# Performance work log

Measured on AMD Instinct MI355X. Metric: run time of the kernel, lower is better.

## Reference

```python
import jax, jax.numpy as jnp
import numpy as np
from functools import partial

H = 128      # hidden size
IN = 86      # lstm input size (66 pose + 20 conditioning)
OUT = 66     # decoded pose dims
STEPS = 15   # rollout steps


def lstm_cell(u, h, c, Wih, Whh, b):
    # PyTorch gate order: i, f, g, o ; b = b_ih + b_hh precombined by caller
    gates = u @ Wih.T + h @ Whh.T + b          # [B, 4H]
    i, f, g, o = jnp.split(gates, 4, axis=-1)
    i = jax.nn.sigmoid(i)
    f = jax.nn.sigmoid(f)
    g = jnp.tanh(g)
    o = jax.nn.sigmoid(o)
    c = f * c + i * g
    h = o * jnp.tanh(c)
    return h, c


def setup_inputs() -> dict:
    key = jax.random.key(0)
    ks = jax.random.split(key, 12)
    B, T = 8192, 50
    k = 1.0 / np.sqrt(H)  # torch default uniform init bound
    u = lambda kk, shp: jax.random.uniform(kk, shp, jnp.float32, -k, k)
    return {
        "x": jax.random.normal(ks[0], (B, T, IN), jnp.float32),
        "Wih0": u(ks[1], (4 * H, IN)),
        "Whh0": u(ks[2], (4 * H, H)),
        "bih0": u(ks[3], (4 * H,)),
        "bhh0": u(ks[4], (4 * H,)),
        "Wih1": u(ks[5], (4 * H, H)),
        "Whh1": u(ks[6], (4 * H, H)),
        "bih1": u(ks[7], (4 * H,)),
        "bhh1": u(ks[8], (4 * H,)),
        "Wd": u(ks[9], (OUT, H)),
        "bd": u(ks[10], (OUT,)),
    }


def reference(x, Wih0, Whh0, bih0, bhh0, Wih1, Whh1, bih1, bhh1, Wd, bd):
    B = x.shape[0]
    b0 = bih0 + bhh0
    b1 = bih1 + bhh1

    def two_layer(state, u):
        h1, c1, h2, c2 = state
        h1, c1 = lstm_cell(u, h1, c1, Wih0, Whh0, b0)
        h2, c2 = lstm_cell(h1, h2, c2, Wih1, Whh1, b1)
        return (h1, c1, h2, c2), h2

    z = jnp.zeros((B, H), x.dtype)
    state0 = (z, z, z, z)

    # encode the history sequence; only final (h, c) matter
    state, _ = jax.lax.scan(lambda s, u: (two_layer(s, u)[0], None),
                            state0, jnp.swapaxes(x, 0, 1))

    cond = x[:, -1, OUT:]  # [B, 20] conditioning, held fixed during rollout

    # first rollout step uses the full last input frame
    state, h2 = two_layer(state, x[:, -1, :])
    pose0 = h2 @ Wd.T + bd  # [B, 66]

    def roll(carry, _):
        state, pose = carry
        u = jnp.concatenate([pose, cond], axis=-1)  # [B, 86]
        state, h2 = two_layer(state, u)
        pose = h2 @ Wd.T + bd
        return (state, pose), pose

    (_, _), rest = jax.lax.scan(roll, (state, pose0), None, length=STEPS - 1)
    # rest: [14, B, 66] -> stack with pose0 along time
    out = jnp.concatenate([pose0[:, None, :], jnp.swapaxes(rest, 0, 1)], axis=1)
    return out  # [B, 15, 66]
```

## Files before the change

### kernel.cpp

```cpp
#include <hip/hip_runtime.h>
#include <cstdint>
#include <cstddef>

#define H_    128
#define IN_   86
#define OUT_  66
#define T_    50
#define B_    8192
#define NPOSE 15

#define K0T 7
#define K1T 8
#define KDT 4
#define NTD 5
#define S0  232
#define S1  264
#define BR  32
#define THR 512
#define RING 16

#define B0P_OFF 0
#define B0P_SZ  (K0T * 32 * 1024)
#define B1P_OFF (B0P_OFF + B0P_SZ)
#define B1P_SZ  (K1T * 32 * 1024)
#define BDP_OFF (B1P_OFF + B1P_SZ)
#define BDP_SZ  (KDT * NTD * 1024)
#define B0P_N (B0P_SZ / 2)
#define B1P_N (B1P_SZ / 2)
#define TOT_N ((B0P_SZ + B1P_SZ + BDP_SZ) / 2)

typedef __attribute__((ext_vector_type(8))) _Float16 hfrag;
typedef __attribute__((ext_vector_type(4))) float   ffrag;

#define MFMA16(AC, AA, BB) \
  AC = __builtin_amdgcn_mfma_f32_16x16x32_f16((AA), (BB), (AC), 0, 0, 0)

template <int N> struct IC { static constexpr int value = N; };
template <int N, class F>
__device__ __forceinline__ void cfor(F&& f) {
  if constexpr (N > 0) {
    cfor<N - 1>(static_cast<F&&>(f));
    f(IC<N - 1>{});
  }
}

template<int MODE>
constexpr int kt_of() { return MODE==0?15: MODE==1?12: MODE==2?8: MODE==3?3: 7; }

template <int N>
__device__ __forceinline__ void waitvm() {
  asm volatile("s_waitcnt vmcnt(%0)" :: "i"(N) : "memory");
}

__device__ __forceinline__ void gload_lds16(const void* g, void* l) {
  __builtin_amdgcn_global_load_lds(
      (const __attribute__((address_space(1))) unsigned int*)g,
      (__attribute__((address_space(3))) unsigned int*)l,
      16, 0, 0);
}

__device__ __forceinline__ unsigned short f16rn(float f) {
  union { _Float16 h; unsigned short u; } cv;
  cv.h = (_Float16)f;
  return cv.u;
}
__device__ __forceinline__ float sigmoid_f(float v) {
  return __fdividef(1.f, 1.f + __expf(-v));
}
__device__ __forceinline__ float tanh_f(float v) {
  float av = fabsf(v);
  float e  = __expf(-2.f * av);
  float t  = __fdividef(1.f - e, 1.f + e);
  return copysignf(t, v);
}

__global__ void wm_prep(
    const float* __restrict__ Wih0, const float* __restrict__ Whh0,
    const float* __restrict__ Wih1, const float* __restrict__ Whh1,
    const float* __restrict__ Wd,
    unsigned short* __restrict__ wsu)
{
  const int idx = blockIdx.x * 256 + threadIdx.x;
  if (idx >= TOT_N) return;
  int region, l;
  if (idx < B0P_N)               { region = 0; l = idx; }
  else if (idx < B0P_N + B1P_N)  { region = 1; l = idx - B0P_N; }
  else                           { region = 2; l = idx - (B0P_N + B1P_N); }

  int k, nt, lane, j;
  if (region < 2) {
    k  = l >> 14;
    int r1 = l & 16383;
    nt = r1 >> 9;
    int li = r1 & 511;
    lane = li >> 3; j = li & 7;
  } else {
    k  = l / 2560;
    int r1 = l % 2560;
    nt = r1 >> 9;
    int li = r1 & 511;
    lane = li >> 3; j = li & 7;
  }
  const int n  = nt * 16 + (lane & 15);
  const int kk = k * 32 + (lane >> 4) * 8 + j;

  float v = 0.f;
  if (region == 0) {
    if (kk < IN_)                    v = Wih0[n * IN_ + kk];
    else if (kk >= 96 && kk < 224)   v = Whh0[n * H_ + (kk - 96)];
  } else if (region == 1) {
    v = (kk < H_) ? Wih1[n * H_ + kk] : Whh1[n * H_ + (kk - H_)];
  } else {
    if (n < OUT_)                    v = Wd[n * H_ + kk];
  }
  wsu[idx] = f16rn(v);
}

__global__ __launch_bounds__(THR, 2) void wm_main(
    const float* __restrict__ x,
    const char*  __restrict__ wsb,
    const float* __restrict__ bih0, const float* __restrict__ bhh0,
    const float* __restrict__ bih1, const float* __restrict__ bhh1,
    const float* __restrict__ bd,
    float* __restrict__ out)
{
  __shared__ __align__(16) unsigned short A0h[BR * S0];
  __shared__ __align__(16) unsigned short A1h[BR * S1];
  __shared__ __align__(16) char RG[8][RING * 1024];

  const int tid  = threadIdx.x;
  const int lane = tid & 63;
  const int uw   = tid >> 6;
  const int ln15 = lane & 15;
  const int quad = lane >> 4;
  const int quad4 = quad * 4;
  const int lane16 = lane * 16;

  const char* B0 = wsb + B0P_OFF;
  const char* B1 = wsb + B1P_OFF;
  const char* BD = wsb + BDP_OFF;
  char* myring = &RG[uw][0];
  const _Float16* A0f = (const _Float16*)A0h;
  const _Float16* A1f = (const _Float16*)A1h;

  for (int i = tid; i < BR * S0; i += THR) A0h[i] = 0;
  for (int i = tid; i < BR * S1; i += THR) A1h[i] = 0;

  float b0r[4], b1r[4];
  #pragma unroll
  for (int g = 0; g < 4; ++g) {
    const int n = g * 128 + uw * 16 + ln15;
    b0r[g] = bih0[n] + bhh0[n];
    b1r[g] = bih1[n] + bhh1[n];
  }
  const int od = uw * 16 + ln15;
  const float bdr = (uw < NTD && od < OUT_) ? bd[od] : 0.f;

  float c1[2][4], c2[2][4];
  #pragma unroll
  for (int m = 0; m < 2; ++m)
    #pragma unroll
    for (int r = 0; r < 4; ++r) { c1[m][r] = 0.f; c2[m][r] = 0.f; }

  const int a0b0 = ln15 * S0 + quad * 8;
  const int a0b1 = (16 + ln15) * S0 + quad * 8;
  const int a1b0 = ln15 * S1 + quad * 8;
  const int a1b1 = (16 + ln15) * S1 + quad * 8;
  const int unit = uw * 16 + ln15;
  const int xr_row = tid >> 4;
  const int xr_col = tid & 15;

  ffrag acc0[2][4], acc1[2][4];

  auto binit0 = [&]() {
    #pragma unroll
    for (int m = 0; m < 2; ++m)
      #pragma unroll
      for (int g = 0; g < 4; ++g) acc0[m][g] = (ffrag){b0r[g], b0r[g], b0r[g], b0r[g]};
  };
  auto binit1 = [&]() {
    #pragma unroll
    for (int m = 0; m < 2; ++m)
      #pragma unroll
      for (int g = 0; g < 4; ++g) acc1[m][g] = (ffrag){b1r[g], b1r[g], b1r[g], b1r[g]};
  };
  auto pw_l1 = [&]() {
    #pragma unroll
    for (int m = 0; m < 2; ++m)
      #pragma unroll
      for (int rr = 0; rr < 4; ++rr) {
        const float ig = sigmoid_f(acc0[m][0][rr]);
        const float fg = sigmoid_f(acc0[m][1][rr]);
        const float gg = tanh_f(acc0[m][2][rr]);
        const float og = sigmoid_f(acc0[m][3][rr]);
        const float c  = fmaf(fg, c1[m][rr], ig * gg);
        c1[m][rr] = c;
        const float h  = og * tanh_f(c);
        const unsigned short hv = f16rn(h);
        const int row = m * 16 + quad4 + rr;
        A0h[row * S0 + 96 + unit] = hv;
        A1h[row * S1 + unit]      = hv;
      }
  };
  auto pw_l2 = [&]() {
    #pragma unroll
    for (int m = 0; m < 2; ++m)
      #pragma unroll
      for (int rr = 0; rr < 4; ++rr) {
        const float ig = sigmoid_f(acc1[m][0][rr]);
        const float fg = sigmoid_f(acc1[m][1][rr]);
        const float gg = tanh_f(acc1[m][2][rr]);
        const float og = sigmoid_f(acc1[m][3][rr]);
        const float c  = fmaf(fg, c2[m][rr], ig * gg);
        c2[m][rr] = c;
        const float h  = og * tanh_f(c);
        const int row = m * 16 + quad4 + rr;
        A1h[row * S1 + 128 + unit] = f16rn(h);
      }
  };

  auto issue_jt = [&](auto mc2, auto jc2) {
    constexpr int MODE = decltype(mc2)::value;
    constexpr int i = decltype(jc2)::value;
    constexpr bool i1 = (MODE <= 2) && (i < K1T);
    constexpr int ik = MODE==0 ? (i1 ? i : i - 8)
                     : MODE==1 ? (i1 ? i : 3 + (i - 8))
                     : i;
    constexpr int ISB = (4 * i) % RING;
    const char* src = (i1 ? B1 : B0) + (size_t)ik * 32 * 1024;
    #pragma unroll
    for (int g = 0; g < 4; ++g)
      gload_lds16(src + (size_t)(g * 8 + uw) * 1024 + lane16,
                  myring + (ISB + g) * 1024);
  };
  auto prefetch_g = [&](auto mc2) {
    constexpr int MODE = decltype(mc2)::value;
    constexpr int NP = kt_of<MODE>() < 4 ? kt_of<MODE>() : 4;
    cfor<NP>([&](auto jc) { issue_jt(mc2, jc); });
  };

  auto run_gemm = [&](auto mc, auto pfc) {
    constexpr int MODE = decltype(mc)::value;
    constexpr bool PF = decltype(pfc)::value != 0;
    constexpr int KT = kt_of<MODE>();
    if constexpr (!PF) prefetch_g(mc);
    cfor<KT>([&](auto jc) {
      constexpr int j = decltype(jc)::value;
      constexpr bool is1 = (MODE <= 2) && (j < K1T);
      constexpr int k = MODE==0 ? (is1 ? j : j - 8)
                      : MODE==1 ? (is1 ? j : 3 + (j - 8))
                      : j;
      constexpr int REM = KT - 1 - j;
      constexpr int W = 4 * (REM < 3 ? REM : 3);
      waitvm<W>();
      hfrag a0, a1;
      if constexpr (is1) {
        a0 = *(const hfrag*)(A1f + a1b0 + k * 32);
        a1 = *(const hfrag*)(A1f + a1b1 + k * 32);
      } else {
        a0 = *(const hfrag*)(A0f + a0b0 + k * 32);
        a1 = *(const hfrag*)(A0f + a0b1 + k * 32);
      }
      constexpr int SB = (4 * j) % RING;
      __builtin_amdgcn_s_setprio(1);
      #pragma unroll
      for (int g = 0; g < 4; ++g) {
        const hfrag bh = *(const hfrag*)(myring + (SB + g) * 1024 + lane16);
        if constexpr (is1) { MFMA16(acc1[0][g], a0, bh); MFMA16(acc1[1][g], a1, bh); }
        else               { MFMA16(acc0[0][g], a0, bh); MFMA16(acc0[1][g], a1, bh); }
      }
      __builtin_amdgcn_s_setprio(0);
      if constexpr (j + 4 < KT) issue_jt(mc, IC<j + 4>{});
    });
  };

  auto barrier2 = [&]() {
    asm volatile("s_waitcnt lgkmcnt(0)" ::: "memory");
    __builtin_amdgcn_s_barrier();
    asm volatile("" ::: "memory");
  };

  barrier2();

  {
    const float* xr = x + ((size_t)(blockIdx.x * BR + xr_row) * T_ + 0) * IN_;
    float xv[6];
    #pragma unroll
    for (int m = 0; m < 6; ++m) {
      const int k = xr_col + m * 16;
      xv[m] = (k < IN_) ? __builtin_nontemporal_load(xr + k) : 0.f;
    }
    #pragma unroll
    for (int m = 0; m < 6; ++m) {
      const int k = xr_col + m * 16;
      if (k < IN_) A0h[xr_row * S0 + k] = f16rn(xv[m]);
    }
  }
  prefetch_g(IC<4>{});
  barrier2();
  binit0();
  run_gemm(IC<4>{}, IC<1>{});
  barrier2();

  for (int t = 0; t < T_; ++t) {
    float xv[6];
    const bool stg = (t < T_ - 1);
    if (stg) {
      const float* xr = x + ((size_t)(blockIdx.x * BR + xr_row) * T_ + (t + 1)) * IN_;
      #pragma unroll
      for (int m = 0; m < 6; ++m) {
        const int k = xr_col + m * 16;
        xv[m] = (k < IN_) ? __builtin_nontemporal_load(xr + k) : 0.f;
      }
      __builtin_amdgcn_sched_barrier(0);
    }
    prefetch_g(IC<0>{});
    if (t > 0) pw_l2();
    pw_l1();
    if (stg) {
      #pragma unroll
      for (int m = 0; m < 6; ++m) {
        const int k = xr_col + m * 16;
        if (k < IN_) A0h[xr_row * S0 + k] = f16rn(xv[m]);
      }
    }
    barrier2();

    binit1();
    binit0();
    run_gemm(IC<0>{}, IC<1>{});
    barrier2();
  }

  for (int t = T_; t < T_ + NPOSE; ++t) {
    const bool more = (t < T_ + NPOSE - 1);
    prefetch_g(IC<2>{});
    if (t == T_) pw_l2();
    pw_l1();
    barrier2();

    binit1();
    if (more) { binit0(); run_gemm(IC<1>{}, IC<1>{}); }
    else      { run_gemm(IC<2>{}, IC<1>{}); }
    barrier2();

    hfrag bdreg[4];
    if (uw < NTD) {
      #pragma unroll
      for (int k = 0; k < KDT; ++k)
        bdreg[k] = *(const hfrag*)(BD + (size_t)(k * NTD + uw) * 1024 + lane16);
    }
    __builtin_amdgcn_sched_barrier(0);
    if (more) prefetch_g(IC<3>{});
    pw_l2();
    barrier2();

    const int s = t - T_;
    if (uw < NTD) {
      ffrag d0 = (ffrag){bdr, bdr, bdr, bdr};
      ffrag d1 = (ffrag){bdr, bdr, bdr, bdr};
      #pragma unroll
      for (int k = 0; k < KDT; ++k) {
        const hfrag ah0 = *(const hfrag*)(A1f + a1b0 + 128 + k * 32);
        const hfrag ah1 = *(const hfrag*)(A1f + a1b1 + 128 + k * 32);
        MFMA16(d0, ah0, bdreg[k]);
        MFMA16(d1, ah1, bdreg[k]);
      }
      if (od < OUT_) {
        #pragma unroll
        for (int m = 0; m < 2; ++m)
          #pragma unroll
          for (int rr = 0; rr < 4; ++rr) {
            const int row = m * 16 + quad4 + rr;
            const float v = m ? d1[rr] : d0[rr];
            __builtin_nontemporal_store(
                v, out + ((size_t)(blockIdx.x * BR + row) * NPOSE + s) * OUT_ + od);
            if (s < NPOSE - 1) A0h[row * S0 + od] = f16rn(v);
          }
      }
    }
    barrier2();

    if (more) run_gemm(IC<3>{}, IC<1>{});
  }
}

extern "C" void kernel_launch(void* const* d_in, const int* in_sizes, int n_in,
                              void* d_out, int out_size, void* d_ws, size_t ws_size,
                              hipStream_t stream)
{
  const float* x    = (const float*)d_in[0];
  const float* Wih0 = (const float*)d_in[1];
  const float* Whh0 = (const float*)d_in[2];
  const float* bih0 = (const float*)d_in[3];
  const float* bhh0 = (const float*)d_in[4];
  const float* Wih1 = (const float*)d_in[5];
  const float* Whh1 = (const float*)d_in[6];
  const float* bih1 = (const float*)d_in[7];
  const float* bhh1 = (const float*)d_in[8];
  const float* Wd   = (const float*)d_in[9];
  const float* bd   = (const float*)d_in[10];

  wm_prep<<<(TOT_N + 255) / 256, 256, 0, stream>>>(Wih0, Whh0, Wih1, Whh1, Wd,
                                                   (unsigned short*)d_ws);
  wm_main<<<B_ / BR, THR, 0, stream>>>(x, (const char*)d_ws,
                                       bih0, bhh0, bih1, bhh1, bd,
                                       (float*)d_out);
}
```

Before: 1.368 ms.

## Stream weight tiles directly into registers instead of an LDS ring

Replaces the per-wave LDS ring filled by async global_load_lds with a register-resident prefetch buffer of three k-tiles loaded by ordinary global loads. This removes the LDS round trip and the manual vmcnt waits, frees a large LDS allocation, and drops the sched_barriers so the compiler schedules the loads itself. The cost is higher VGPR pressure under launch bounds of two blocks per CU, a shallower prefetch depth, and waits on loads placed by the compiler.

```diff
diff --git a/kernel.cpp b/kernel.cpp
--- a/kernel.cpp
+++ b/kernel.cpp
@@ -17,7 +17,7 @@
 #define S1  264
 #define BR  32
 #define THR 512
-#define RING 16
+#define PF  3
 
 #define B0P_OFF 0
 #define B0P_SZ  (K0T * 32 * 1024)
@@ -46,18 +46,6 @@
 
 template<int MODE>
 constexpr int kt_of() { return MODE==0?15: MODE==1?12: MODE==2?8: MODE==3?3: 7; }
-
-template <int N>
-__device__ __forceinline__ void waitvm() {
-  asm volatile("s_waitcnt vmcnt(%0)" :: "i"(N) : "memory");
-}
-
-__device__ __forceinline__ void gload_lds16(const void* g, void* l) {
-  __builtin_amdgcn_global_load_lds(
-      (const __attribute__((address_space(1))) unsigned int*)g,
-      (__attribute__((address_space(3))) unsigned int*)l,
-      16, 0, 0);
-}
 
 __device__ __forceinline__ unsigned short f16rn(float f) {
   union { _Float16 h; unsigned short u; } cv;
@@ -126,7 +114,6 @@
 {
   __shared__ __align__(16) unsigned short A0h[BR * S0];
   __shared__ __align__(16) unsigned short A1h[BR * S1];
-  __shared__ __align__(16) char RG[8][RING * 1024];
 
   const int tid  = threadIdx.x;
   const int lane = tid & 63;
@@ -139,7 +126,6 @@
   const char* B0 = wsb + B0P_OFF;
   const char* B1 = wsb + B1P_OFF;
   const char* BD = wsb + BDP_OFF;
-  char* myring = &RG[uw][0];
   const _Float16* A0f = (const _Float16*)A0h;
   const _Float16* A1f = (const _Float16*)A1h;
 
@@ -171,6 +157,7 @@
   const int xr_col = tid & 15;
 
   ffrag acc0[2][4], acc1[2][4];
+  hfrag bp[PF][4];
 
   auto binit0 = [&]() {
     #pragma unroll
@@ -226,33 +213,30 @@
     constexpr int ik = MODE==0 ? (i1 ? i : i - 8)
                      : MODE==1 ? (i1 ? i : 3 + (i - 8))
                      : i;
-    constexpr int ISB = (4 * i) % RING;
+    constexpr int SLOT = i % PF;
     const char* src = (i1 ? B1 : B0) + (size_t)ik * 32 * 1024;
     #pragma unroll
     for (int g = 0; g < 4; ++g)
-      gload_lds16(src + (size_t)(g * 8 + uw) * 1024 + lane16,
-                  myring + (ISB + g) * 1024);
+      bp[SLOT][g] = *(const hfrag*)(src + (size_t)(g * 8 + uw) * 1024 + lane16);
   };
   auto prefetch_g = [&](auto mc2) {
     constexpr int MODE = decltype(mc2)::value;
-    constexpr int NP = kt_of<MODE>() < 4 ? kt_of<MODE>() : 4;
+    constexpr int NP = kt_of<MODE>() < PF ? kt_of<MODE>() : PF;
     cfor<NP>([&](auto jc) { issue_jt(mc2, jc); });
   };
 
   auto run_gemm = [&](auto mc, auto pfc) {
     constexpr int MODE = decltype(mc)::value;
-    constexpr bool PF = decltype(pfc)::value != 0;
+    constexpr bool PFD = decltype(pfc)::value != 0;
     constexpr int KT = kt_of<MODE>();
-    if constexpr (!PF) prefetch_g(mc);
+    if constexpr (!PFD) prefetch_g(mc);
     cfor<KT>([&](auto jc) {
       constexpr int j = decltype(jc)::value;
       constexpr bool is1 = (MODE <= 2) && (j < K1T);
       constexpr int k = MODE==0 ? (is1 ? j : j - 8)
                       : MODE==1 ? (is1 ? j : 3 + (j - 8))
                       : j;
-      constexpr int REM = KT - 1 - j;
-      constexpr int W = 4 * (REM < 3 ? REM : 3);
-      waitvm<W>();
+      constexpr int SLOT = j % PF;
       hfrag a0, a1;
       if constexpr (is1) {
         a0 = *(const hfrag*)(A1f + a1b0 + k * 32);
@@ -261,16 +245,14 @@
         a0 = *(const hfrag*)(A0f + a0b0 + k * 32);
         a1 = *(const hfrag*)(A0f + a0b1 + k * 32);
       }
-      constexpr int SB = (4 * j) % RING;
       __builtin_amdgcn_s_setprio(1);
       #pragma unroll
       for (int g = 0; g < 4; ++g) {
-        const hfrag bh = *(const hfrag*)(myring + (SB + g) * 1024 + lane16);
-        if constexpr (is1) { MFMA16(acc1[0][g], a0, bh); MFMA16(acc1[1][g], a1, bh); }
-        else               { MFMA16(acc0[0][g], a0, bh); MFMA16(acc0[1][g], a1, bh); }
+        if constexpr (is1) { MFMA16(acc1[0][g], a0, bp[SLOT][g]); MFMA16(acc1[1][g], a1, bp[SLOT][g]); }
+        else               { MFMA16(acc0[0][g], a0, bp[SLOT][g]); MFMA16(acc0[1][g], a1, bp[SLOT][g]); }
       }
       __builtin_amdgcn_s_setprio(0);
-      if constexpr (j + 4 < KT) issue_jt(mc, IC<j + 4>{});
+      if constexpr (j + PF < KT) issue_jt(mc, IC<j + PF>{});
     });
   };
 
@@ -312,7 +294,6 @@
         const int k = xr_col + m * 16;
         xv[m] = (k < IN_) ? __builtin_nontemporal_load(xr + k) : 0.f;
       }
-      __builtin_amdgcn_sched_barrier(0);
     }
     prefetch_g(IC<0>{});
     if (t > 0) pw_l2();
@@ -350,7 +331,6 @@
       for (int k = 0; k < KDT; ++k)
         bdreg[k] = *(const hfrag*)(BD + (size_t)(k * NTD + uw) * 1024 + lane16);
     }
-    __builtin_amdgcn_sched_barrier(0);
     if (more) prefetch_g(IC<3>{});
     pw_l2();
     barrier2();
```

Result: slower. 1.752 ms (+28.1%).

## Keep six layer-1 weight k-tiles resident in registers across timesteps

Applied to the files above, without the earlier changes.

Loads the first six k-tiles of the packed layer-1 weights into per-thread registers once, before the timestep loop. Each GEMM then runs those tiles straight from registers and streams only the remaining tiles through the LDS ring. Prefetch depth and ring size shrink from 4 to 3 stages, and two sched_barriers are removed. The aim is to cut global/L2 weight traffic and LDS ring pressure on every step, at the cost of 48 extra VGPRs per thread, which may lower occupancy or cause spills.

```diff
diff --git a/kernel.cpp b/kernel.cpp
--- a/kernel.cpp
+++ b/kernel.cpp
@@ -13,11 +13,12 @@
 #define K1T 8
 #define KDT 4
 #define NTD 5
+#define NW1 6
 #define S0  232
 #define S1  264
 #define BR  32
 #define THR 512
-#define RING 16
+#define RING 12
 
 #define B0P_OFF 0
 #define B0P_SZ  (K0T * 32 * 1024)
@@ -44,8 +45,18 @@
   }
 }
 
-template<int MODE>
-constexpr int kt_of() { return MODE==0?15: MODE==1?12: MODE==2?8: MODE==3?3: 7; }
+template<int MODE> constexpr int ns_of() {
+  return MODE==0?9: MODE==1?6: MODE==2?2: MODE==3?3: 7;
+}
+template<int MODE, int J> constexpr bool s_is1() {
+  return (MODE==0||MODE==1) ? (J<2) : (MODE==2);
+}
+template<int MODE, int J> constexpr int s_k() {
+  return MODE==0 ? (J<2 ? 6+J : J-2)
+       : MODE==1 ? (J<2 ? 6+J : J+1)
+       : MODE==2 ? 6+J
+       : J;
+}
 
 template <int N>
 __device__ __forceinline__ void waitvm() {
@@ -146,6 +157,14 @@
   for (int i = tid; i < BR * S0; i += THR) A0h[i] = 0;
   for (int i = tid; i < BR * S1; i += THR) A1h[i] = 0;
 
+  hfrag w1[NW1][4];
+  cfor<NW1>([&](auto kc) {
+    constexpr int kt = decltype(kc)::value;
+    #pragma unroll
+    for (int g = 0; g < 4; ++g)
+      w1[kt][g] = *(const hfrag*)(B1 + (size_t)((kt * 32 + g * 8 + uw) * 1024) + lane16);
+  });
+
   float b0r[4], b1r[4];
   #pragma unroll
   for (int g = 0; g < 4; ++g) {
@@ -222,10 +241,8 @@
   auto issue_jt = [&](auto mc2, auto jc2) {
     constexpr int MODE = decltype(mc2)::value;
     constexpr int i = decltype(jc2)::value;
-    constexpr bool i1 = (MODE <= 2) && (i < K1T);
-    constexpr int ik = MODE==0 ? (i1 ? i : i - 8)
-                     : MODE==1 ? (i1 ? i : 3 + (i - 8))
-                     : i;
+    constexpr bool i1 = s_is1<MODE, i>();
+    constexpr int ik = s_k<MODE, i>();
     constexpr int ISB = (4 * i) % RING;
     const char* src = (i1 ? B1 : B0) + (size_t)ik * 32 * 1024;
     #pragma unroll
@@ -235,42 +252,52 @@
   };
   auto prefetch_g = [&](auto mc2) {
     constexpr int MODE = decltype(mc2)::value;
-    constexpr int NP = kt_of<MODE>() < 4 ? kt_of<MODE>() : 4;
+    constexpr int NP = ns_of<MODE>() < 3 ? ns_of<MODE>() : 3;
     cfor<NP>([&](auto jc) { issue_jt(mc2, jc); });
   };
 
-  auto run_gemm = [&](auto mc, auto pfc) {
+  auto run_gemm = [&](auto mc) {
     constexpr int MODE = decltype(mc)::value;
-    constexpr bool PF = decltype(pfc)::value != 0;
-    constexpr int KT = kt_of<MODE>();
-    if constexpr (!PF) prefetch_g(mc);
-    cfor<KT>([&](auto jc) {
+    constexpr int NS = ns_of<MODE>();
+    if constexpr (MODE <= 2) {
+      cfor<NW1>([&](auto kc) {
+        constexpr int kt = decltype(kc)::value;
+        const hfrag a0 = *(const hfrag*)(A1f + a1b0 + kt * 32);
+        const hfrag a1v = *(const hfrag*)(A1f + a1b1 + kt * 32);
+        __builtin_amdgcn_s_setprio(1);
+        #pragma unroll
+        for (int g = 0; g < 4; ++g) {
+          MFMA16(acc1[0][g], a0, w1[kt][g]);
+          MFMA16(acc1[1][g], a1v, w1[kt][g]);
+        }
+        __builtin_amdgcn_s_setprio(0);
+      });
+    }
+    cfor<NS>([&](auto jc) {
       constexpr int j = decltype(jc)::value;
-      constexpr bool is1 = (MODE <= 2) && (j < K1T);
-      constexpr int k = MODE==0 ? (is1 ? j : j - 8)
-                      : MODE==1 ? (is1 ? j : 3 + (j - 8))
-                      : j;
-      constexpr int REM = KT - 1 - j;
-      constexpr int W = 4 * (REM < 3 ? REM : 3);
+      constexpr bool is1 = s_is1<MODE, j>();
+      constexpr int k = s_k<MODE, j>();
+      constexpr int REM = NS - 1 - j;
+      constexpr int W = 4 * (REM < 2 ? REM : 2);
       waitvm<W>();
-      hfrag a0, a1;
+      hfrag a0, a1v;
       if constexpr (is1) {
-        a0 = *(const hfrag*)(A1f + a1b0 + k * 32);
-        a1 = *(const hfrag*)(A1f + a1b1 + k * 32);
+        a0  = *(const hfrag*)(A1f + a1b0 + k * 32);
+        a1v = *(const hfrag*)(A1f + a1b1 + k * 32);
       } else {
-        a0 = *(const hfrag*)(A0f + a0b0 + k * 32);
-        a1 = *(const hfrag*)(A0f + a0b1 + k * 32);
+        a0  = *(const hfrag*)(A0f + a0b0 + k * 32);
+        a1v = *(const hfrag*)(A0f + a0b1 + k * 32);
       }
       constexpr int SB = (4 * j) % RING;
       __builtin_amdgcn_s_setprio(1);
       #pragma unroll
       for (int g = 0; g < 4; ++g) {
         const hfrag bh = *(const hfrag*)(myring + (SB + g) * 1024 + lane16);
-        if constexpr (is1) { MFMA16(acc1[0][g], a0, bh); MFMA16(acc1[1][g], a1, bh); }
-        else               { MFMA16(acc0[0][g], a0, bh); MFMA16(acc0[1][g], a1, bh); }
+        if constexpr (is1) { MFMA16(acc1[0][g], a0, bh); MFMA16(acc1[1][g], a1v, bh); }
+        else               { MFMA16(acc0[0][g], a0, bh); MFMA16(acc0[1][g], a1v, bh); }
       }
       __builtin_amdgcn_s_setprio(0);
-      if constexpr (j + 4 < KT) issue_jt(mc, IC<j + 4>{});
+      if constexpr (j + 3 < NS) issue_jt(mc, IC<j + 3>{});
     });
   };
 
@@ -299,7 +326,7 @@
   prefetch_g(IC<4>{});
   barrier2();
   binit0();
-  run_gemm(IC<4>{}, IC<1>{});
+  run_gemm(IC<4>{});
   barrier2();
 
   for (int t = 0; t < T_; ++t) {
@@ -312,7 +339,6 @@
         const int k = xr_col + m * 16;
         xv[m] = (k < IN_) ? __builtin_nontemporal_load(xr + k) : 0.f;
       }
-      __builtin_amdgcn_sched_barrier(0);
     }
     prefetch_g(IC<0>{});
     if (t > 0) pw_l2();
@@ -328,20 +354,21 @@
 
     binit1();
     binit0();
-    run_gemm(IC<0>{}, IC<1>{});
+    run_gemm(IC<0>{});
     barrier2();
   }
 
   for (int t = T_; t < T_ + NPOSE; ++t) {
     const bool more = (t < T_ + NPOSE - 1);
-    prefetch_g(IC<2>{});
+    if (more) prefetch_g(IC<1>{});
+    else      prefetch_g(IC<2>{});
     if (t == T_) pw_l2();
     pw_l1();
     barrier2();
 
     binit1();
-    if (more) { binit0(); run_gemm(IC<1>{}, IC<1>{}); }
-    else      { run_gemm(IC<2>{}, IC<1>{}); }
+    if (more) { binit0(); run_gemm(IC<1>{}); }
+    else      { run_gemm(IC<2>{}); }
     barrier2();
 
     hfrag bdreg[4];
@@ -350,7 +377,6 @@
       for (int k = 0; k < KDT; ++k)
         bdreg[k] = *(const hfrag*)(BD + (size_t)(k * NTD + uw) * 1024 + lane16);
     }
-    __builtin_amdgcn_sched_barrier(0);
     if (more) prefetch_g(IC<3>{});
     pw_l2();
     barrier2();
@@ -381,7 +407,7 @@
     }
     barrier2();
 
-    if (more) run_gemm(IC<3>{}, IC<1>{});
+    if (more) run_gemm(IC<3>{});
   }
 }
 
```

New measurement: 1.698 ms. +24.1%, slower.
